# Performance work log

Hardware: AMD Instinct MI355X
Metric: run time of the kernel (lower is better)

Reference implementation:

```python
import jax, jax.numpy as jnp
import numpy as np

B, T, T2, C, H = 8, 1024, 257, 1024, 16
D = C // H          # head dim = 64
HID = 256           # global adapter hidden_size
SCALE = 1.0 / np.sqrt(D).astype(np.float32)


def _ln(x, g, b, eps=1e-5):
    mu = jnp.mean(x, -1, keepdims=True)
    var = jnp.mean(jnp.square(x - mu), -1, keepdims=True)
    return (x - mu) * jax.lax.rsqrt(var + eps) * g + b


def setup_inputs() -> dict:
    key = jax.random.key(0)
    ks = jax.random.split(key, 32)
    w = lambda k, shape: jax.random.normal(k, shape, jnp.float32) * 0.02
    inp = {
        'x': jax.random.normal(ks[0], (B, T, C), jnp.float32),
        'enc_x': jax.random.normal(ks[1], (B, T2, C), jnp.float32),
        'ln1_g': jnp.ones((C,), jnp.float32), 'ln1_b': jnp.zeros((C,), jnp.float32),
        'ln2_g': jnp.ones((C,), jnp.float32), 'ln2_b': jnp.zeros((C,), jnp.float32),
        'ln3_g': jnp.ones((C,), jnp.float32), 'ln3_b': jnp.zeros((C,), jnp.float32),
        'attn_qkv_w': w(ks[2], (C, 3 * C)), 'attn_qkv_b': jnp.zeros((3 * C,), jnp.float32),
        'attn_proj_w': w(ks[3], (C, C)), 'attn_proj_b': jnp.zeros((C,), jnp.float32),
        'ca_q_w': w(ks[4], (C, C)), 'ca_q_b': jnp.zeros((C,), jnp.float32),
        'ca_k_w': w(ks[5], (C, C)), 'ca_k_b': jnp.zeros((C,), jnp.float32),
        'ca_v_w': w(ks[6], (C, C)), 'ca_v_b': jnp.zeros((C,), jnp.float32),
        'ca_proj_w': w(ks[7], (C, C)), 'ca_proj_b': jnp.zeros((C,), jnp.float32),
        'fc_w': w(ks[8], (C, 4 * C)), 'fc_b': jnp.zeros((4 * C,), jnp.float32),
        'mlp_proj_w': w(ks[9], (4 * C, C)), 'mlp_proj_b': jnp.zeros((C,), jnp.float32),
        'ad_down_w': w(ks[10], (C, HID)), 'ad_down_b': jnp.zeros((HID,), jnp.float32),
        'ad_up_w': w(ks[11], (HID, C)), 'ad_up_b': jnp.zeros((C,), jnp.float32),
    }
    return inp


def _heads(t, n_tok):  # [B, n_tok, C] -> [B, H, n_tok, D]
    return t.reshape(B, n_tok, H, D).transpose(0, 2, 1, 3)


def _block(x, enc_x, ln1_g, ln1_b, ln2_g, ln2_b, ln3_g, ln3_b,
           attn_qkv_w, attn_qkv_b, attn_proj_w, attn_proj_b,
           ca_q_w, ca_q_b, ca_k_w, ca_k_b, ca_v_w, ca_v_b, ca_proj_w, ca_proj_b,
           fc_w, fc_b, mlp_proj_w, mlp_proj_b,
           ad_down_w, ad_down_b, ad_up_w, ad_up_b):
    # --- causal self-attention ---
    h = _ln(x, ln1_g, ln1_b)
    qkv = h @ attn_qkv_w + attn_qkv_b
    q, k, v = jnp.split(qkv, 3, axis=-1)
    q, k, v = _heads(q, T), _heads(k, T), _heads(v, T)
    att = jnp.einsum('bhtd,bhsd->bhts', q, k) * SCALE
    causal = jnp.tril(jnp.ones((T, T), bool))
    att = jax.nn.softmax(jnp.where(causal, att, -jnp.inf), axis=-1)
    o = jnp.einsum('bhts,bhsd->bthd', att, v).reshape(B, T, C)
    x = x + o @ attn_proj_w + attn_proj_b
    # --- cross-attention (no mask) ---
    h = _ln(x, ln3_g, ln3_b)
    q = _heads(h @ ca_q_w + ca_q_b, T)
    k = _heads(enc_x @ ca_k_w + ca_k_b, T2)
    v = _heads(enc_x @ ca_v_w + ca_v_b, T2)
    att = jax.nn.softmax(jnp.einsum('bhtd,bhsd->bhts', q, k) * SCALE, axis=-1)
    o = jnp.einsum('bhts,bhsd->bthd', att, v).reshape(B, T, C)
    x = x + o @ ca_proj_w + ca_proj_b
    # --- MLP ---
    h = _ln(x, ln2_g, ln2_b)
    x = x + jax.nn.gelu(h @ fc_w + fc_b, approximate=True) @ mlp_proj_w + mlp_proj_b
    # --- adapter (residual inside) ---
    a = jax.nn.relu(x @ ad_down_w + ad_down_b) @ ad_up_w + ad_up_b
    return a + x


def reference(x, enc_x, ln1_g, ln1_b, ln2_g, ln2_b, ln3_g, ln3_b,
              attn_qkv_w, attn_qkv_b, attn_proj_w, attn_proj_b,
              ca_q_w, ca_q_b, ca_k_w, ca_k_b, ca_v_w, ca_v_b, ca_proj_w, ca_proj_b,
              fc_w, fc_b, mlp_proj_w, mlp_proj_b,
              ad_down_w, ad_down_b, ad_up_w, ad_up_b):
    out = _block(x, enc_x, ln1_g, ln1_b, ln2_g, ln2_b, ln3_g, ln3_b,
                 attn_qkv_w, attn_qkv_b, attn_proj_w, attn_proj_b,
                 ca_q_w, ca_q_b, ca_k_w, ca_k_b, ca_v_w, ca_v_b, ca_proj_w, ca_proj_b,
                 fc_w, fc_b, mlp_proj_w, mlp_proj_b,
                 ad_down_w, ad_down_b, ad_up_w, ad_up_b)
    return (out, enc_x)
```

## Files before the change

kernel.cpp:

```cpp
#include <hip/hip_runtime.h>

typedef unsigned short UST;
typedef __attribute__((ext_vector_type(8))) short short8;
typedef __attribute__((ext_vector_type(4))) float f32x4;
typedef __attribute__((ext_vector_type(4))) unsigned short us4;

#define DEV __device__ __forceinline__

DEV float b2f(UST u){ union{unsigned int i; float f;} x; x.i=((unsigned int)u)<<16; return x.f; }
DEV UST f2b(float f){ union{float f; unsigned int i;} x; x.f=f; return (UST)((x.i + 0x7FFFu + ((x.i>>16)&1u))>>16); }
DEV float ldf(const void* p, size_t i, int fl){ return fl ? b2f(((const UST*)p)[i]) : ((const float*)p)[i]; }

DEV void g2l16(const UST* g, UST* l){
  __builtin_amdgcn_global_load_lds((const __attribute__((address_space(1))) unsigned int*)g,
                                   (__attribute__((address_space(3))) unsigned int*)l, 16, 0, 0);
}

__global__ __launch_bounds__(256) void detect_k(const unsigned int* __restrict__ x, int* __restrict__ flag)
{
  int tid = threadIdx.x;
  int cnt = 0;
#pragma unroll
  for (int j=0;j<4;j++){
    unsigned e = (x[tid*4+j] >> 7) & 0xFF;
    cnt += (e >= 100 && e <= 140) ? 1 : 0;
  }
  __shared__ int tot;
  if (tid==0) tot = 0;
  __syncthreads();
  atomicAdd(&tot, cnt);
  __syncthreads();
  if (tid==0) flag[0] = (tot > 512) ? 1 : 0;
}

template<int EPI, bool MTAIL>
__global__ __launch_bounds__(256) void gemm128(
    const UST* __restrict__ A, const UST* __restrict__ Bt, const void* __restrict__ bias,
    int M, int N, int K,
    UST* __restrict__ out, float* __restrict__ resid, void* __restrict__ aux,
    const int* __restrict__ flag)
{
  __shared__ UST As[128*32];
  __shared__ UST Bs[128*32];
  const int fl = flag[0];
  int tid = threadIdx.x;
  int bx = blockIdx.x, by = blockIdx.y;
  int lane = tid & 63, w = tid >> 6;
  int wr = w >> 1, wc = w & 1;
  int lr = lane & 15, lk = (lane >> 4) << 3;

  int c0 = tid, c1 = tid + 256;
  int ar0 = by*128 + (c0>>2), ar1 = by*128 + (c1>>2);
  if (MTAIL){ ar0 = ar0 < M ? ar0 : M-1; ar1 = ar1 < M ? ar1 : M-1; }
  int br0 = bx*128 + (c0>>2), br1 = bx*128 + (c1>>2);
  int ak0 = (c0&3)<<3, ak1 = (c1&3)<<3;
  const UST* pa0 = A + (size_t)ar0*K + ak0;
  const UST* pa1 = A + (size_t)ar1*K + ak1;
  const UST* pb0 = Bt + (size_t)br0*K + ak0;
  const UST* pb1 = Bt + (size_t)br1*K + ak1;
  UST* la0 = &As[c0*8]; UST* la1 = &As[c1*8];
  UST* lb0 = &Bs[c0*8]; UST* lb1 = &Bs[c1*8];

  f32x4 acc[4][4] = {};

  for (int k0 = 0; k0 < K; k0 += 32){
    g2l16(pa0, la0); g2l16(pa1, la1);
    g2l16(pb0, lb0); g2l16(pb1, lb1);
    pa0 += 32; pa1 += 32; pb0 += 32; pb1 += 32;
    __syncthreads();
    short8 af[4], bf[4];
#pragma unroll
    for (int m=0;m<4;m++) af[m] = *(const short8*)&As[(wr*64 + m*16 + lr)*32 + lk];
#pragma unroll
    for (int n=0;n<4;n++) bf[n] = *(const short8*)&Bs[(wc*64 + n*16 + lr)*32 + lk];
#pragma unroll
    for (int m=0;m<4;m++)
#pragma unroll
      for (int n=0;n<4;n++)
        acc[m][n] = __builtin_amdgcn_mfma_f32_16x16x32_bf16(af[m], bf[n], acc[m][n], 0,0,0);
    __syncthreads();
  }

  float bv[4];
#pragma unroll
  for (int n=0;n<4;n++) bv[n] = ldf(bias, bx*128 + wc*64 + n*16 + lr, fl);
#pragma unroll
  for (int m=0;m<4;m++){
#pragma unroll
    for (int r=0;r<4;r++){
      int gr = by*128 + wr*64 + m*16 + ((lane>>4)<<2) + r;
      if (MTAIL && gr >= M) continue;
#pragma unroll
      for (int n=0;n<4;n++){
        int gc = bx*128 + wc*64 + n*16 + lr;
        float v = acc[m][n][r] + bv[n];
        size_t idx = (size_t)gr*N + gc;
        if (EPI == 0){ out[idx] = f2b(v); }
        else if (EPI == 1){ float e = __expf(-1.5957691216f*(v + 0.044715f*v*v*v)); out[idx] = f2b(v/(1.f+e)); }
        else if (EPI == 2){ out[idx] = f2b(v > 0.f ? v : 0.f); }
        else if (EPI == 3){ resid[idx] += v; }
        else if (EPI == 4){ float x2 = resid[idx] + v; resid[idx] = x2; ((UST*)aux)[idx] = f2b(x2); }
        else { float x2 = resid[idx] + v; if (fl) ((UST*)aux)[idx] = f2b(x2); else ((float*)aux)[idx] = x2; }
      }
    }
  }
}

__global__ __launch_bounds__(256) void ln_k(const float* __restrict__ xf, const void* __restrict__ g,
                                            const void* __restrict__ b, UST* __restrict__ out,
                                            const int* __restrict__ flag)
{
  const int fl = flag[0];
  int row = blockIdx.x, tid = threadIdx.x;
  const float* xr = xf + (size_t)row*1024;
  f32x4 v = *(const f32x4*)&xr[tid*4];
  float s = v[0]+v[1]+v[2]+v[3];
  float ss = v[0]*v[0]+v[1]*v[1]+v[2]*v[2]+v[3]*v[3];
#pragma unroll
  for (int off=32; off>0; off>>=1){ s += __shfl_down(s, off); ss += __shfl_down(ss, off); }
  __shared__ float sm[8];
  int w = tid>>6;
  if ((tid&63)==0){ sm[w] = s; sm[4+w] = ss; }
  __syncthreads();
  s = sm[0]+sm[1]+sm[2]+sm[3];
  ss = sm[4]+sm[5]+sm[6]+sm[7];
  float mu = s*(1.f/1024.f);
  float rs = rsqrtf(ss*(1.f/1024.f) - mu*mu + 1e-5f);
  us4 o;
#pragma unroll
  for (int j=0;j<4;j++){
    int c = tid*4+j;
    o[j] = f2b((v[j]-mu)*rs*ldf(g,c,fl) + ldf(b,c,fl));
  }
  *(us4*)&out[(size_t)row*1024 + tid*4] = o;
}

#define NEGBIG (-1e30f)
template<bool CAUSAL>
__global__ __launch_bounds__(256) void attn2(
    const UST* __restrict__ Qb, size_t qB, int qT,
    const UST* __restrict__ Kb, size_t kB, int kT,
    const UST* __restrict__ Vt, int vS,
    UST* __restrict__ O, int nk)
{
  __shared__ UST Ks[2][4096];
  __shared__ UST Vs[2][4096];
  __shared__ UST plds[4][16][72];

  int p = blockIdx.x, bh = blockIdx.y;
  int b = bh >> 4, h = bh & 15;
  int tid = threadIdx.x, w = tid >> 6, lane = tid & 63;
  int lr = lane & 15;
  const UST* q0 = Qb + (size_t)b*qB + h*64;
  const UST* kp = Kb + (size_t)b*kB + h*64;
  const UST* vp = Vt + (size_t)bh*64*vS;
  const int skmax = nk - 1;

  auto stageK = [&](int bufi, int s0){
#pragma unroll
    for (int it=0; it<2; it++){
      int c = tid + it*256;
      int s = c >> 3;
      int srcb = ((c & 7) << 4) ^ ((s & 7) << 4);
      int sg = s0 + s; sg = sg <= skmax ? sg : skmax;
      g2l16(kp + (size_t)sg*kT + (srcb>>1), &Ks[bufi][c*8]);
    }
  };
  auto stageV = [&](int bufi, int s0){
#pragma unroll
    for (int it=0; it<2; it++){
      int c = tid + it*256;
      int d = c >> 3;
      int srcb = ((c & 7) << 4) ^ ((d & 7) << 4);
      g2l16(vp + (size_t)d*vS + s0 + (srcb>>1), &Vs[bufi][c*8]);
    }
  };

  int qtiles[2]; int nq;
  if (CAUSAL){ qtiles[0] = 15 - p; qtiles[1] = p; nq = 2; }
  else       { qtiles[0] = p; nq = 1; }

  for (int qi=0; qi<nq; qi++){
    int qt = qtiles[qi];
    int t0 = qt*64 + w*16;
    int qr0 = t0 + ((lane>>4)<<2);
    short8 qf0 = *(const short8*)&q0[(size_t)(t0+lr)*qT + ((lane>>4)<<3)];
    short8 qf1 = *(const short8*)&q0[(size_t)(t0+lr)*qT + 32 + ((lane>>4)<<3)];
    f32x4 oacc[4] = {};
    float m[4], l[4];
#pragma unroll
    for (int r=0;r<4;r++){ m[r] = NEGBIG; l[r] = 0.f; }

    int nt = CAUSAL ? (qt + 1) : ((nk + 63) >> 6);
    int cur = 0;
    stageK(0, 0); stageV(0, 0);
    __syncthreads();

    for (int t=0; t<nt; t++){
      int s0 = t*64;
      int nxt = cur ^ 1;
      if (t+1 < nt){ stageK(nxt, s0 + 64); stageV(nxt, s0 + 64); }

      f32x4 sf[4];
      const char* ksb = (const char*)&Ks[cur][0];
      __builtin_amdgcn_s_setprio(1);
#pragma unroll
      for (int hf=0; hf<4; hf++){
        int r = hf*16 + lr;
        int sw = (r & 7) << 4;
        int lo = (lane >> 4) << 4;
        short8 k0 = *(const short8*)(ksb + r*128 + (lo ^ sw));
        short8 k1 = *(const short8*)(ksb + r*128 + ((64 + lo) ^ sw));
        f32x4 s_ = {};
        s_ = __builtin_amdgcn_mfma_f32_16x16x32_bf16(qf0, k0, s_, 0,0,0);
        s_ = __builtin_amdgcn_mfma_f32_16x16x32_bf16(qf1, k1, s_, 0,0,0);
        sf[hf] = s_;
      }
      __builtin_amdgcn_s_setprio(0);

      bool needMask = (CAUSAL && (s0+63 > t0)) || (s0+63 >= nk);
#pragma unroll
      for (int hf=0; hf<4; hf++)
#pragma unroll
        for (int r=0;r<4;r++){
          float sv = sf[hf][r]*0.125f;
          if (needMask){
            int key = s0 + hf*16 + lr;
            if ((CAUSAL && key > qr0 + r) || key >= nk) sv = NEGBIG;
          }
          sf[hf][r] = sv;
        }

      float mx[4];
#pragma unroll
      for (int r=0;r<4;r++) mx[r] = fmaxf(fmaxf(sf[0][r], sf[1][r]), fmaxf(sf[2][r], sf[3][r]));
#pragma unroll
      for (int off=1; off<16; off<<=1)
#pragma unroll
        for (int r=0;r<4;r++) mx[r] = fmaxf(mx[r], __shfl_xor(mx[r], off));
      float scl[4];
#pragma unroll
      for (int r=0;r<4;r++){
        float mn = fmaxf(m[r], mx[r]);
        scl[r] = __expf(m[r] - mn);
        m[r] = mn;
      }
#pragma unroll
      for (int hf=0; hf<4; hf++)
#pragma unroll
        for (int r=0;r<4;r++){
          float d = sf[hf][r] - m[r];
          sf[hf][r] = (d < -80.f) ? 0.f : __expf(d);
        }
      float sum[4];
#pragma unroll
      for (int r=0;r<4;r++) sum[r] = (sf[0][r] + sf[1][r]) + (sf[2][r] + sf[3][r]);
#pragma unroll
      for (int off=1; off<16; off<<=1)
#pragma unroll
        for (int r=0;r<4;r++) sum[r] += __shfl_xor(sum[r], off);
#pragma unroll
      for (int r=0;r<4;r++) l[r] = l[r]*scl[r] + sum[r];
#pragma unroll
      for (int nf=0;nf<4;nf++)
#pragma unroll
        for (int r=0;r<4;r++) oacc[nf][r] *= scl[r];

#pragma unroll
      for (int hf=0; hf<4; hf++)
#pragma unroll
        for (int r=0;r<4;r++)
          plds[w][((lane>>4)<<2)+r][hf*16+lr] = f2b(sf[hf][r]);

      const char* pb = (const char*)&plds[w][0][0];
      short8 pf0 = *(const short8*)(pb + lr*144 +      ((lane>>4)<<4));
      short8 pf1 = *(const short8*)(pb + lr*144 + 64 + ((lane>>4)<<4));

      const char* vsb = (const char*)&Vs[cur][0];
      __builtin_amdgcn_s_setprio(1);
#pragma unroll
      for (int nf=0; nf<4; nf++){
        int d = nf*16 + lr;
        int sw = (d & 7) << 4;
        int lo = (lane >> 4) << 4;
        short8 vf0 = *(const short8*)(vsb + d*128 + (lo ^ sw));
        short8 vf1 = *(const short8*)(vsb + d*128 + ((64 + lo) ^ sw));
        oacc[nf] = __builtin_amdgcn_mfma_f32_16x16x32_bf16(pf0, vf0, oacc[nf], 0,0,0);
        oacc[nf] = __builtin_amdgcn_mfma_f32_16x16x32_bf16(pf1, vf1, oacc[nf], 0,0,0);
      }
      __builtin_amdgcn_s_setprio(0);

      __syncthreads();
      cur = nxt;
    }

#pragma unroll
    for (int nf=0;nf<4;nf++)
#pragma unroll
      for (int r=0;r<4;r++){
        int t = t0 + ((lane>>4)<<2) + r;
        O[(size_t)(b*1024 + t)*1024 + h*64 + nf*16 + lr] = f2b(oacc[nf][r] / l[r]);
      }
  }
}

__global__ __launch_bounds__(256) void transposeW(const void* __restrict__ in, UST* __restrict__ out,
                                                  int K, int N, const int* __restrict__ flag)
{
  const int fl = flag[0];
  int n0 = blockIdx.x*64, k0 = blockIdx.y*64;
  __shared__ UST t[64][72];
  int tid = threadIdx.x;
  int r = tid>>3, cc = (tid&7)*8;
#pragma unroll
  for (int it=0; it<2; it++){
    int k = r + it*32;
    short8 v;
    if (fl){
      v = *(const short8*)&((const UST*)in)[(size_t)(k0+k)*N + n0 + cc];
    } else {
      const float* inf = (const float*)in;
      f32x4 a = *(const f32x4*)&inf[(size_t)(k0+k)*N + n0 + cc];
      f32x4 b = *(const f32x4*)&inf[(size_t)(k0+k)*N + n0 + cc + 4];
#pragma unroll
      for (int j=0;j<4;j++){ v[j] = (short)f2b(a[j]); v[4+j] = (short)f2b(b[j]); }
    }
    *(short8*)&t[k][cc] = v;
  }
  __syncthreads();
#pragma unroll
  for (int it=0; it<2; it++){
    int n = r + it*32;
    short8 v;
#pragma unroll
    for (int j=0;j<8;j++) v[j] = t[cc+j][n];
    *(short8*)&out[(size_t)(n0+n)*K + k0 + cc] = v;
  }
}

__global__ __launch_bounds__(256) void transposeVself(const UST* __restrict__ qkv, UST* __restrict__ vt)
{
  int t0 = blockIdx.x*64; int bh = blockIdx.y; int b = bh>>4, h = bh&15;
  __shared__ UST t[64][72];
  int tid = threadIdx.x, r = tid>>3, cc = (tid&7)*8;
#pragma unroll
  for (int it=0; it<2; it++){
    int tt = r + it*32;
    short8 v = *(const short8*)&qkv[((size_t)(b*1024 + t0 + tt))*3072 + 2048 + h*64 + cc];
    *(short8*)&t[tt][cc] = v;
  }
  __syncthreads();
#pragma unroll
  for (int it=0; it<2; it++){
    int d = r + it*32;
    short8 v;
#pragma unroll
    for (int j=0;j<8;j++) v[j] = t[cc+j][d];
    *(short8*)&vt[((size_t)(bh*64 + d))*1024 + t0 + cc] = v;
  }
}

__global__ __launch_bounds__(256) void transposeVcross(const UST* __restrict__ v2, UST* __restrict__ vt2)
{
  int s0 = blockIdx.x*64; int bh = blockIdx.y; int b = bh>>4, h = bh&15;
  __shared__ UST t[64][72];
  int tid = threadIdx.x, r = tid>>3, cc = (tid&7)*8;
#pragma unroll
  for (int it=0; it<2; it++){
    int s = s0 + r + it*32; if (s > 256) s = 256;
    short8 v = *(const short8*)&v2[((size_t)(b*257 + s))*1024 + h*64 + cc];
    *(short8*)&t[r+it*32][cc] = v;
  }
  __syncthreads();
#pragma unroll
  for (int it=0; it<2; it++){
    int d = r + it*32;
#pragma unroll
    for (int j=0;j<8;j++){
      int s = s0 + cc + j;
      if (s < 257) vt2[((size_t)(bh*64 + d))*288 + s] = t[cc+j][d];
    }
  }
}

__global__ __launch_bounds__(256) void cvt_f32(const void* __restrict__ in, float* __restrict__ out,
                                               const int* __restrict__ flag)
{
  const int fl = flag[0];
  size_t i = ((size_t)blockIdx.x*256 + threadIdx.x)*4;
  f32x4 o;
  if (fl){
    us4 v = *(const us4*)&((const UST*)in)[i];
#pragma unroll
    for (int j=0;j<4;j++) o[j] = b2f(v[j]);
  } else {
    o = *(const f32x4*)&((const float*)in)[i];
  }
  *(f32x4*)&out[i] = o;
}

__global__ __launch_bounds__(256) void encpass(const void* __restrict__ in, UST* __restrict__ enc_c,
                                               void* __restrict__ outp, const int* __restrict__ flag)
{
  const int fl = flag[0];
  size_t i = ((size_t)blockIdx.x*256 + threadIdx.x)*4;
  if (fl){
    us4 v = *(const us4*)&((const UST*)in)[i];
    *(us4*)&enc_c[i] = v;
    *(us4*)&((UST*)outp)[8388608 + i] = v;
  } else {
    f32x4 v = *(const f32x4*)&((const float*)in)[i];
    us4 c;
#pragma unroll
    for (int j=0;j<4;j++) c[j] = f2b(v[j]);
    *(us4*)&enc_c[i] = c;
    *(f32x4*)&((float*)outp)[8388608 + i] = v;
  }
}

extern "C" void kernel_launch(void* const* d_in, const int* in_sizes, int n_in,
                              void* d_out, int out_size, void* d_ws, size_t ws_size,
                              hipStream_t stream) {
  (void)in_sizes; (void)n_in; (void)out_size; (void)ws_size;
  const void* x       = d_in[0];
  const void* enc     = d_in[1];
  const void* ln1g    = d_in[2];
  const void* ln1b    = d_in[3];
  const void* ln2g    = d_in[4];
  const void* ln2b    = d_in[5];
  const void* ln3g    = d_in[6];
  const void* ln3b    = d_in[7];
  const void* qkvW    = d_in[8];
  const void* qkvB    = d_in[9];
  const void* projW   = d_in[10];
  const void* projB   = d_in[11];
  const void* caqW    = d_in[12];
  const void* caqB    = d_in[13];
  const void* cakW    = d_in[14];
  const void* cakB    = d_in[15];
  const void* cavW    = d_in[16];
  const void* cavB    = d_in[17];
  const void* caprojW = d_in[18];
  const void* caprojB = d_in[19];
  const void* fcW     = d_in[20];
  const void* fcB     = d_in[21];
  const void* mlpW    = d_in[22];
  const void* mlpB    = d_in[23];
  const void* adwW    = d_in[24];
  const void* adwB    = d_in[25];
  const void* aupW    = d_in[26];
  const void* aupB    = d_in[27];

  unsigned char* ws = (unsigned char*)d_ws;
  int*   flag = (int*)ws;
  float* xf   = (float*)(ws + 256);
  UST*   big  = (UST*)(ws + 33554688);
  UST*   h    = (UST*)(ws + 100663552);
  UST*   o    = (UST*)(ws + 117440768);
  UST*   wT   = (UST*)(ws + 134217984);
  UST*   encc = (UST*)(ws + 168820992);
  UST* qkvT    = wT;
  UST* projT   = wT + 3145728;
  UST* caqT    = wT + 4194304;
  UST* cakT    = wT + 5242880;
  UST* cavT    = wT + 6291456;
  UST* caprojT = wT + 7340032;
  UST* fcT     = wT + 8388608;
  UST* mlpT    = wT + 12582912;
  UST* adwT    = wT + 16777216;
  UST* aupT    = wT + 17039360;
  UST* q2  = big;
  UST* k2  = big + 8388608;
  UST* v2  = big + 10493952;
  UST* vtX = big + 25165824;

  detect_k<<<1,256,0,stream>>>((const unsigned int*)x, flag);

  transposeW<<<dim3(48,16),256,0,stream>>>(qkvW,    qkvT,    1024, 3072, flag);
  transposeW<<<dim3(16,16),256,0,stream>>>(projW,   projT,   1024, 1024, flag);
  transposeW<<<dim3(16,16),256,0,stream>>>(caqW,    caqT,    1024, 1024, flag);
  transposeW<<<dim3(16,16),256,0,stream>>>(cakW,    cakT,    1024, 1024, flag);
  transposeW<<<dim3(16,16),256,0,stream>>>(cavW,    cavT,    1024, 1024, flag);
  transposeW<<<dim3(16,16),256,0,stream>>>(caprojW, caprojT, 1024, 1024, flag);
  transposeW<<<dim3(64,16),256,0,stream>>>(fcW,     fcT,     1024, 4096, flag);
  transposeW<<<dim3(16,64),256,0,stream>>>(mlpW,    mlpT,    4096, 1024, flag);
  transposeW<<<dim3(4,16), 256,0,stream>>>(adwW,    adwT,    1024, 256,  flag);
  transposeW<<<dim3(16,4), 256,0,stream>>>(aupW,    aupT,    256,  1024, flag);

  cvt_f32<<<8192,256,0,stream>>>(x, xf, flag);
  encpass<<<2056,256,0,stream>>>(enc, encc, d_out, flag);

  ln_k<<<8192,256,0,stream>>>(xf, ln1g, ln1b, h, flag);
  gemm128<0,false><<<dim3(24,64),256,0,stream>>>(h, qkvT, qkvB, 8192, 3072, 1024, big, nullptr, nullptr, flag);
  transposeVself<<<dim3(16,128),256,0,stream>>>(big, vtX);
  attn2<true><<<dim3(8,128),256,0,stream>>>(big, (size_t)1024*3072, 3072,
                                            big+1024, (size_t)1024*3072, 3072,
                                            vtX, 1024, o, 1024);
  gemm128<3,false><<<dim3(8,64),256,0,stream>>>(o, projT, projB, 8192, 1024, 1024, nullptr, xf, nullptr, flag);

  ln_k<<<8192,256,0,stream>>>(xf, ln3g, ln3b, h, flag);
  gemm128<0,false><<<dim3(8,64),256,0,stream>>>(h, caqT, caqB, 8192, 1024, 1024, q2, nullptr, nullptr, flag);
  gemm128<0,true ><<<dim3(8,17),256,0,stream>>>(encc, cakT, cakB, 2056, 1024, 1024, k2, nullptr, nullptr, flag);
  gemm128<0,true ><<<dim3(8,17),256,0,stream>>>(encc, cavT, cavB, 2056, 1024, 1024, v2, nullptr, nullptr, flag);
  transposeVcross<<<dim3(5,128),256,0,stream>>>(v2, vtX);
  attn2<false><<<dim3(16,128),256,0,stream>>>(q2, (size_t)1024*1024, 1024,
                                              k2, (size_t)257*1024, 1024,
                                              vtX, 288, o, 257);
  gemm128<3,false><<<dim3(8,64),256,0,stream>>>(o, caprojT, caprojB, 8192, 1024, 1024, nullptr, xf, nullptr, flag);

  ln_k<<<8192,256,0,stream>>>(xf, ln2g, ln2b, h, flag);
  gemm128<1,false><<<dim3(32,64),256,0,stream>>>(h, fcT, fcB, 8192, 4096, 1024, big, nullptr, nullptr, flag);
  gemm128<4,false><<<dim3(8,64),256,0,stream>>>(big, mlpT, mlpB, 8192, 1024, 4096, nullptr, xf, h, flag);

  gemm128<2,false><<<dim3(2,64),256,0,stream>>>(h, adwT, adwB, 8192, 256, 1024, o, nullptr, nullptr, flag);
  gemm128<5,false><<<dim3(8,64),256,0,stream>>>(o, aupT, aupB, 8192, 1024, 256, nullptr, xf, d_out, flag);
}
```

Measured before the change: 930.4 us.

## Double-buffer GEMM LDS tiles and remap blocks across XCDs for L2 reuse

The GEMM kernel now uses two LDS buffers so the next K-tile's global-to-LDS loads are issued before the current tile's MFMAs, keeping one barrier per iteration. Launches become 1D, and block ids are remapped so consecutive tiles on the same XCD share weight columns, improving L2 locality. MFMA sections are wrapped with s_setprio. LDS use doubles, which may reduce occupancy, and the barrier's wait on outstanding loads may limit the overlap.

```diff
diff --git a/kernel.cpp b/kernel.cpp
--- a/kernel.cpp
+++ b/kernel.cpp
@@ -36,15 +36,20 @@
 template<int EPI, bool MTAIL>
 __global__ __launch_bounds__(256) void gemm128(
     const UST* __restrict__ A, const UST* __restrict__ Bt, const void* __restrict__ bias,
-    int M, int N, int K,
+    int M, int N, int K, int gy,
     UST* __restrict__ out, float* __restrict__ resid, void* __restrict__ aux,
     const int* __restrict__ flag)
 {
-  __shared__ UST As[128*32];
-  __shared__ UST Bs[128*32];
+  __shared__ UST As[2][128*32];
+  __shared__ UST Bs[2][128*32];
   const int fl = flag[0];
   int tid = threadIdx.x;
-  int bx = blockIdx.x, by = blockIdx.y;
+
+  int nwg = gridDim.x;
+  int cpx = nwg >> 3;
+  int o = (blockIdx.x & 7)*cpx + (blockIdx.x >> 3);
+  int bx = o / gy, by = o % gy;
+
   int lane = tid & 63, w = tid >> 6;
   int wr = w >> 1, wc = w & 1;
   int lr = lane & 15, lk = (lane >> 4) << 3;
@@ -58,27 +63,36 @@
   const UST* pa1 = A + (size_t)ar1*K + ak1;
   const UST* pb0 = Bt + (size_t)br0*K + ak0;
   const UST* pb1 = Bt + (size_t)br1*K + ak1;
-  UST* la0 = &As[c0*8]; UST* la1 = &As[c1*8];
-  UST* lb0 = &Bs[c0*8]; UST* lb1 = &Bs[c1*8];
 
   f32x4 acc[4][4] = {};
 
-  for (int k0 = 0; k0 < K; k0 += 32){
-    g2l16(pa0, la0); g2l16(pa1, la1);
-    g2l16(pb0, lb0); g2l16(pb1, lb1);
-    pa0 += 32; pa1 += 32; pb0 += 32; pb1 += 32;
-    __syncthreads();
+  int nt = K >> 5;
+  g2l16(pa0, &As[0][c0*8]); g2l16(pa1, &As[0][c1*8]);
+  g2l16(pb0, &Bs[0][c0*8]); g2l16(pb1, &Bs[0][c1*8]);
+  __syncthreads();
+
+  int cur = 0;
+  for (int t = 0; t < nt; t++){
+    int nxt = cur ^ 1;
+    if (t+1 < nt){
+      int ko = (t+1) << 5;
+      g2l16(pa0 + ko, &As[nxt][c0*8]); g2l16(pa1 + ko, &As[nxt][c1*8]);
+      g2l16(pb0 + ko, &Bs[nxt][c0*8]); g2l16(pb1 + ko, &Bs[nxt][c1*8]);
+    }
     short8 af[4], bf[4];
 #pragma unroll
-    for (int m=0;m<4;m++) af[m] = *(const short8*)&As[(wr*64 + m*16 + lr)*32 + lk];
-#pragma unroll
-    for (int n=0;n<4;n++) bf[n] = *(const short8*)&Bs[(wc*64 + n*16 + lr)*32 + lk];
+    for (int m=0;m<4;m++) af[m] = *(const short8*)&As[cur][(wr*64 + m*16 + lr)*32 + lk];
+#pragma unroll
+    for (int n=0;n<4;n++) bf[n] = *(const short8*)&Bs[cur][(wc*64 + n*16 + lr)*32 + lk];
+    __builtin_amdgcn_s_setprio(1);
 #pragma unroll
     for (int m=0;m<4;m++)
 #pragma unroll
       for (int n=0;n<4;n++)
         acc[m][n] = __builtin_amdgcn_mfma_f32_16x16x32_bf16(af[m], bf[n], acc[m][n], 0,0,0);
+    __builtin_amdgcn_s_setprio(0);
     __syncthreads();
+    cur = nxt;
   }
 
   float bv[4];
@@ -491,27 +505,27 @@
   encpass<<<2056,256,0,stream>>>(enc, encc, d_out, flag);
 
   ln_k<<<8192,256,0,stream>>>(xf, ln1g, ln1b, h, flag);
-  gemm128<0,false><<<dim3(24,64),256,0,stream>>>(h, qkvT, qkvB, 8192, 3072, 1024, big, nullptr, nullptr, flag);
+  gemm128<0,false><<<24*64,256,0,stream>>>(h, qkvT, qkvB, 8192, 3072, 1024, 64, big, nullptr, nullptr, flag);
   transposeVself<<<dim3(16,128),256,0,stream>>>(big, vtX);
   attn2<true><<<dim3(8,128),256,0,stream>>>(big, (size_t)1024*3072, 3072,
                                             big+1024, (size_t)1024*3072, 3072,
                                             vtX, 1024, o, 1024);
-  gemm128<3,false><<<dim3(8,64),256,0,stream>>>(o, projT, projB, 8192, 1024, 1024, nullptr, xf, nullptr, flag);
+  gemm128<3,false><<<8*64,256,0,stream>>>(o, projT, projB, 8192, 1024, 1024, 64, nullptr, xf, nullptr, flag);
 
   ln_k<<<8192,256,0,stream>>>(xf, ln3g, ln3b, h, flag);
-  gemm128<0,false><<<dim3(8,64),256,0,stream>>>(h, caqT, caqB, 8192, 1024, 1024, q2, nullptr, nullptr, flag);
-  gemm128<0,true ><<<dim3(8,17),256,0,stream>>>(encc, cakT, cakB, 2056, 1024, 1024, k2, nullptr, nullptr, flag);
-  gemm128<0,true ><<<dim3(8,17),256,0,stream>>>(encc, cavT, cavB, 2056, 1024, 1024, v2, nullptr, nullptr, flag);
+  gemm128<0,false><<<8*64,256,0,stream>>>(h, caqT, caqB, 8192, 1024, 1024, 64, q2, nullptr, nullptr, flag);
+  gemm128<0,true ><<<8*17,256,0,stream>>>(encc, cakT, cakB, 2056, 1024, 1024, 17, k2, nullptr, nullptr, flag);
+  gemm128<0,true ><<<8*17,256,0,stream>>>(encc, cavT, cavB, 2056, 1024, 1024, 17, v2, nullptr, nullptr, flag);
   transposeVcross<<<dim3(5,128),256,0,stream>>>(v2, vtX);
   attn2<false><<<dim3(16,128),256,0,stream>>>(q2, (size_t)1024*1024, 1024,
                                               k2, (size_t)257*1024, 1024,
                                               vtX, 288, o, 257);
-  gemm128<3,false><<<dim3(8,64),256,0,stream>>>(o, caprojT, caprojB, 8192, 1024, 1024, nullptr, xf, nullptr, flag);
+  gemm128<3,false><<<8*64,256,0,stream>>>(o, caprojT, caprojB, 8192, 1024, 1024, 64, nullptr, xf, nullptr, flag);
 
   ln_k<<<8192,256,0,stream>>>(xf, ln2g, ln2b, h, flag);
-  gemm128<1,false><<<dim3(32,64),256,0,stream>>>(h, fcT, fcB, 8192, 4096, 1024, big, nullptr, nullptr, flag);
-  gemm128<4,false><<<dim3(8,64),256,0,stream>>>(big, mlpT, mlpB, 8192, 1024, 4096, nullptr, xf, h, flag);
-
-  gemm128<2,false><<<dim3(2,64),256,0,stream>>>(h, adwT, adwB, 8192, 256, 1024, o, nullptr, nullptr, flag);
-  gemm128<5,false><<<dim3(8,64),256,0,stream>>>(o, aupT, aupB, 8192, 1024, 256, nullptr, xf, d_out, flag);
-}
+  gemm128<1,false><<<32*64,256,0,stream>>>(h, fcT, fcB, 8192, 4096, 1024, 64, big, nullptr, nullptr, flag);
+  gemm128<4,false><<<8*64,256,0,stream>>>(big, mlpT, mlpB, 8192, 1024, 4096, 64, nullptr, xf, h, flag);
+
+  gemm128<2,false><<<2*64,256,0,stream>>>(h, adwT, adwB, 8192, 256, 1024, 64, o, nullptr, nullptr, flag);
+  gemm128<5,false><<<8*64,256,0,stream>>>(o, aupT, aupB, 8192, 1024, 256, 64, nullptr, xf, d_out, flag);
+}
```

After: 902.9 us. -3.0%, faster.
